# Optimization experiments

Hardware: AMD Instinct MI355X
Metric: run time of the kernel (lower is better)

Reference implementation:

```python
import jax, jax.numpy as jnp
import numpy as np

B, T, C = 1, 2048, 1024
H = 16
D = C // H
FF = 4 * C


def layernorm(x, g, b, eps=1e-5):
    mu = jnp.mean(x, axis=-1, keepdims=True)
    var = jnp.var(x, axis=-1, keepdims=True)
    return (x - mu) * jax.lax.rsqrt(var + eps) * g + b


def setup_inputs() -> dict:
    key = jax.random.key(0)
    ks = jax.random.split(key, 16)
    s = 0.02
    return {
        "x": jax.random.normal(ks[0], (B, T, C), jnp.float32),
        "qkv_w": jax.random.normal(ks[1], (C, 3 * C), jnp.float32) * s,
        "qkv_b": jnp.zeros((3 * C,), jnp.float32),
        "out_w": jax.random.normal(ks[2], (C, C), jnp.float32) * s,
        "out_b": jnp.zeros((C,), jnp.float32),
        "ln1_g": jnp.ones((C,), jnp.float32),
        "ln1_b": jnp.zeros((C,), jnp.float32),
        "ln2_g": jnp.ones((C,), jnp.float32),
        "ln2_b": jnp.zeros((C,), jnp.float32),
        "w1": jax.random.normal(ks[3], (C, FF), jnp.float32) * s,
        "b1": jnp.zeros((FF,), jnp.float32),
        "w2": jax.random.normal(ks[4], (FF, C), jnp.float32) * s,
        "b2": jnp.zeros((C,), jnp.float32),
    }


def linear_attention(h, qkv_w, qkv_b, out_w, out_b):
    qkv = h @ qkv_w + qkv_b                      # (B,T,3C)
    q, k, v = jnp.split(qkv, 3, axis=-1)
    # (B,T,C) -> (B,H,T,D)
    reshape = lambda a: a.reshape(B, T, H, D).transpose(0, 2, 1, 3)
    q, k, v = reshape(q), reshape(k), reshape(v)
    Q = jax.nn.elu(q) + 1.0
    K = jax.nn.elu(k) + 1.0
    # causal linear attention via cumulative outer-products
    KV = jnp.einsum('bhtd,bhte->bhtde', K, v)    # (B,H,T,D,D)
    KV_cum = jnp.cumsum(KV, axis=2)
    K_cum = jnp.cumsum(K, axis=2)
    num = jnp.einsum('bhtd,bhtde->bhte', Q, KV_cum)
    den = jnp.einsum('bhtd,bhtd->bht', Q, K_cum)[..., None]
    o = num / (den + 1e-6)                       # (B,H,T,D)
    o = o.transpose(0, 2, 1, 3).reshape(B, T, C)
    return o @ out_w + out_b


def reference(x, qkv_w, qkv_b, out_w, out_b, ln1_g, ln1_b, ln2_g, ln2_b, w1, b1, w2, b2):
    x = x + linear_attention(layernorm(x, ln1_g, ln1_b), qkv_w, qkv_b, out_w, out_b)
    h = layernorm(x, ln2_g, ln2_b)
    mlp = jax.nn.gelu(h @ w1 + b1, approximate=False) @ w2 + b2
    return x + mlp
```

## Files before the change

kernel.cpp:

```cpp
#include <hip/hip_runtime.h>

typedef unsigned short u16;
typedef __bf16 bf16x8 __attribute__((ext_vector_type(8)));
typedef float f32x4 __attribute__((ext_vector_type(4)));
typedef unsigned short u16x8 __attribute__((ext_vector_type(8)));
typedef unsigned short u16x4 __attribute__((ext_vector_type(4)));

__device__ __forceinline__ float bf2f(u16 u){
  union { unsigned i; float f; } v; v.i = ((unsigned)u) << 16; return v.f;
}
__device__ __forceinline__ u16 f2bf(float f){
  union { float f; unsigned i; } v; v.f = f;
  unsigned r = v.i + 0x7FFFu + ((v.i >> 16) & 1u);
  return (u16)(r >> 16);
}
__device__ __forceinline__ float elup(float x){ return x > 0.f ? x + 1.f : expf(x); }

__device__ __forceinline__ void gload_lds16(const void* gsrc, void* ldst){
  __builtin_amdgcn_global_load_lds(
      (__attribute__((address_space(1))) void*)(unsigned long long)gsrc,
      (__attribute__((address_space(3))) void*)(unsigned)(unsigned long long)ldst,
      16, 0, 0);
}

struct TD { const float* in; u16* out; int R, Cc, cx, ntiles; };

__global__ __launch_bounds__(256) void prep(TD d0, TD d1, TD d2, TD d3,
                                            const float* __restrict__ x, const float* __restrict__ g,
                                            const float* __restrict__ b, u16* __restrict__ y){
  __shared__ u16 tile[32][33];
  __shared__ float ls[4], ls2[4];
  int bidx = blockIdx.x, tid = threadIdx.x;
  if (bidx >= 12288){
    int row = bidx - 12288;
    size_t base = (size_t)row*1024 + tid*4;
    f32x4 xv = *(const f32x4*)(x + base);
    float v0=xv[0], v1=xv[1], v2=xv[2], v3=xv[3];
    float s  = v0+v1+v2+v3;
    float s2 = v0*v0+v1*v1+v2*v2+v3*v3;
    #pragma unroll
    for (int off=32; off>0; off>>=1){ s += __shfl_xor(s, off); s2 += __shfl_xor(s2, off); }
    if ((tid & 63) == 0){ ls[tid>>6] = s; ls2[tid>>6] = s2; }
    __syncthreads();
    float ts = ls[0]+ls[1]+ls[2]+ls[3];
    float ts2 = ls2[0]+ls2[1]+ls2[2]+ls2[3];
    float mean = ts*(1.f/1024.f);
    float var  = ts2*(1.f/1024.f) - mean*mean;
    float rstd = rsqrtf(var + 1e-5f);
    f32x4 gv = *(const f32x4*)(g + tid*4);
    f32x4 bv = *(const f32x4*)(b + tid*4);
    u16x4 ov;
    ov[0]=f2bf((v0-mean)*rstd*gv[0]+bv[0]);
    ov[1]=f2bf((v1-mean)*rstd*gv[1]+bv[1]);
    ov[2]=f2bf((v2-mean)*rstd*gv[2]+bv[2]);
    ov[3]=f2bf((v3-mean)*rstd*gv[3]+bv[3]);
    *(u16x4*)(y + base) = ov;
    return;
  }
  int bb = bidx;
  TD d;
  if (bb < d0.ntiles) d = d0;
  else { bb -= d0.ntiles;
    if (bb < d1.ntiles) d = d1;
    else { bb -= d1.ntiles;
      if (bb < d2.ntiles) d = d2;
      else { bb -= d2.ntiles; d = d3; } } }
  int c0 = (bb % d.cx) * 32, r0 = (bb / d.cx) * 32;
  int tx = tid & 31, ty = tid >> 5;
  #pragma unroll
  for (int i=0;i<4;i++)
    tile[ty + i*8][tx] = f2bf(d.in[(size_t)(r0 + ty + i*8)*d.Cc + c0 + tx]);
  __syncthreads();
  #pragma unroll
  for (int i=0;i<4;i++)
    d.out[(size_t)(c0 + ty + i*8)*d.R + r0 + tx] = tile[tx][ty + i*8];
}

__global__ __launch_bounds__(256) void ln2_fused(const u16* __restrict__ P0, const u16* __restrict__ P1,
                                                 const u16* __restrict__ P2, const u16* __restrict__ P3,
                                                 const float* __restrict__ bias, const float* __restrict__ xres,
                                                 const float* __restrict__ g, const float* __restrict__ b,
                                                 float* __restrict__ x2, u16* __restrict__ h2){
  int row = blockIdx.x, tid = threadIdx.x;
  size_t base = (size_t)row*1024 + tid*4;
  u16x4 a0 = *(const u16x4*)(P0 + base);
  u16x4 a1 = *(const u16x4*)(P1 + base);
  u16x4 a2 = *(const u16x4*)(P2 + base);
  u16x4 a3 = *(const u16x4*)(P3 + base);
  f32x4 rv = *(const f32x4*)(xres + base);
  f32x4 bv = *(const f32x4*)(bias + tid*4);
  f32x4 v;
  #pragma unroll
  for (int j=0;j<4;j++) v[j] = (bf2f(a0[j])+bf2f(a1[j])) + (bf2f(a2[j])+bf2f(a3[j])) + bv[j] + rv[j];
  *(f32x4*)(x2 + base) = v;
  float s  = v[0]+v[1]+v[2]+v[3];
  float s2 = v[0]*v[0]+v[1]*v[1]+v[2]*v[2]+v[3]*v[3];
  #pragma unroll
  for (int off=32; off>0; off>>=1){ s += __shfl_xor(s, off); s2 += __shfl_xor(s2, off); }
  __shared__ float ls[4], ls2[4];
  if ((tid & 63) == 0){ ls[tid>>6] = s; ls2[tid>>6] = s2; }
  __syncthreads();
  float ts = ls[0]+ls[1]+ls[2]+ls[3];
  float ts2 = ls2[0]+ls2[1]+ls2[2]+ls2[3];
  float mean = ts*(1.f/1024.f);
  float var  = ts2*(1.f/1024.f) - mean*mean;
  float rstd = rsqrtf(var + 1e-5f);
  f32x4 gv = *(const f32x4*)(g + tid*4);
  f32x4 bb = *(const f32x4*)(b + tid*4);
  u16x4 ov;
  #pragma unroll
  for (int j=0;j<4;j++) ov[j] = f2bf((v[j]-mean)*rstd*gv[j]+bb[j]);
  *(u16x4*)(h2 + base) = ov;
}

template<int EPI>
__global__ __launch_bounds__(512, 4) void gemm_bt(const u16* __restrict__ A, const u16* __restrict__ BT,
                                                  const float* __restrict__ bias, const float* __restrict__ res,
                                                  void* __restrict__ out, int N, int K, size_t pstride){
  __shared__ u16 As[2][128*64];
  __shared__ u16 Bs[2][128*64];
  int tid = threadIdx.x;
  int w = tid >> 6, lane = tid & 63;
  int m0 = blockIdx.x * 128, n0 = blockIdx.y * 128;
  int Kc = K / gridDim.z;
  int kbase = blockIdx.z * Kc;
  int nt = Kc / 64;

  f32x4 acc[2][4] = {};

  int l3 = lane >> 3, l7 = lane & 7;
  const u16* aSrc = A  + (size_t)(m0 + w*16 + l3)*K + kbase + (l7 ^ l3)*8;
  const u16* bSrc = BT + (size_t)(n0 + w*16 + l3)*K + kbase + (l7 ^ l3)*8;
  int r0 = (w>>1)*32, c0 = (w&1)*64;
  int lrow = lane & 15, g4 = lane >> 4;
  int swz = (lrow & 7) << 4;

  {
    u16* aD = As[0] + w*16*64;
    u16* bD = Bs[0] + w*16*64;
    gload_lds16(aSrc,                aD);
    gload_lds16(aSrc + (size_t)8*K,  aD + 8*64);
    gload_lds16(bSrc,                bD);
    gload_lds16(bSrc + (size_t)8*K,  bD + 8*64);
  }
  __syncthreads();

  int cur = 0;
  for (int t = 0; t < nt; ++t){
    if (t + 1 < nt){
      int k0 = (t+1)*64;
      u16* aD = As[cur^1] + w*16*64;
      u16* bD = Bs[cur^1] + w*16*64;
      gload_lds16(aSrc + k0,               aD);
      gload_lds16(aSrc + (size_t)8*K + k0, aD + 8*64);
      gload_lds16(bSrc + k0,               bD);
      gload_lds16(bSrc + (size_t)8*K + k0, bD + 8*64);
    }
    const char* Ab = (const char*)As[cur];
    const char* Bb = (const char*)Bs[cur];
    #pragma unroll
    for (int kk=0; kk<2; kk++){
      int ko = (kk*64 + g4*16) ^ swz;
      bf16x8 af[2], bfv[4];
      #pragma unroll
      for (int mi=0;mi<2;mi++) af[mi]  = *(const bf16x8*)(Ab + (r0 + mi*16 + lrow)*128 + ko);
      #pragma unroll
      for (int ni=0;ni<4;ni++) bfv[ni] = *(const bf16x8*)(Bb + (c0 + ni*16 + lrow)*128 + ko);
      #pragma unroll
      for (int mi=0;mi<2;mi++)
        #pragma unroll
        for (int ni=0;ni<4;ni++)
          acc[mi][ni] = __builtin_amdgcn_mfma_f32_16x16x32_bf16(af[mi], bfv[ni], acc[mi][ni], 0, 0, 0);
    }
    __syncthreads();
    cur ^= 1;
  }

  int lgr = lane >> 4;
  u16* pout = (EPI == 3) ? ((u16*)out + (size_t)blockIdx.z * pstride) : (u16*)out;
  #pragma unroll
  for (int mi=0;mi<2;mi++){
    #pragma unroll
    for (int j=0;j<4;j++){
      int row = m0 + r0 + mi*16 + lgr*4 + j;
      #pragma unroll
      for (int ni=0;ni<4;ni++){
        int col = n0 + c0 + ni*16 + lrow;
        size_t idx = (size_t)row*N + col;
        if constexpr (EPI == 3){
          pout[idx] = f2bf(acc[mi][ni][j]);
        } else {
          float v = acc[mi][ni][j] + bias[col];
          if constexpr (EPI == 0){
            ((u16*)out)[idx] = f2bf(v);
          } else {
            v = 0.5f * v * (1.f + erff(v * 0.70710678118654752f));
            ((u16*)out)[idx] = f2bf(v);
          }
        }
      }
    }
  }
}

__global__ __launch_bounds__(256) void reduce4(const u16* __restrict__ P0, const u16* __restrict__ P1,
                                               const u16* __restrict__ P2, const u16* __restrict__ P3,
                                               const float* __restrict__ bias, const float* __restrict__ res,
                                               float* __restrict__ out){
  size_t i = ((size_t)blockIdx.x*256 + threadIdx.x)*4;
  u16x4 a = *(const u16x4*)(P0 + i);
  u16x4 b = *(const u16x4*)(P1 + i);
  u16x4 c = *(const u16x4*)(P2 + i);
  u16x4 d = *(const u16x4*)(P3 + i);
  f32x4 rv = *(const f32x4*)(res + i);
  f32x4 bv = *(const f32x4*)(bias + (i & 1023));
  f32x4 o;
  #pragma unroll
  for (int j=0;j<4;j++) o[j] = (bf2f(a[j]) + bf2f(b[j])) + (bf2f(c[j]) + bf2f(d[j])) + bv[j] + rv[j];
  *(f32x4*)(out + i) = o;
}

__global__ __launch_bounds__(256) void attn_chunksum(const u16* __restrict__ qkv, float* __restrict__ S,
                                                     float* __restrict__ Ks){
  __shared__ u16 KT[64*72];
  __shared__ u16 VT[64*72];
  int c = blockIdx.x, h = blockIdx.y, tid = threadIdx.x;
  int t = tid >> 2, seg = tid & 3, e0 = seg*16;
  size_t rowb = (size_t)(c*64 + t)*3072 + h*64 + e0;
  u16x8 k0 = *(const u16x8*)(qkv + rowb + 1024);
  u16x8 k1 = *(const u16x8*)(qkv + rowb + 1032);
  u16x8 v0 = *(const u16x8*)(qkv + rowb + 2048);
  u16x8 v1 = *(const u16x8*)(qkv + rowb + 2056);
  #pragma unroll
  for (int i=0;i<8;i++){
    KT[(e0 + i)*72 + t]     = f2bf(elup(bf2f(k0[i])));
    KT[(e0 + 8 + i)*72 + t] = f2bf(elup(bf2f(k1[i])));
    VT[(e0 + i)*72 + t]     = v0[i];
    VT[(e0 + 8 + i)*72 + t] = v1[i];
  }
  __syncthreads();

  int w = tid >> 6, lane = tid & 63;
  int lr = lane & 15, lk = (lane>>4)*8, g = lane >> 4, cl = lane & 15;
  bf16x8 av_[2];
  #pragma unroll
  for (int kk=0;kk<2;kk++) av_[kk] = *(const bf16x8*)(VT + (w*16 + lr)*72 + kk*32 + lk);
  f32x4 acc[4] = {};
  #pragma unroll
  for (int di=0;di<4;di++){
    #pragma unroll
    for (int kk=0;kk<2;kk++){
      bf16x8 bk = *(const bf16x8*)(KT + (di*16 + lr)*72 + kk*32 + lk);
      acc[di] = __builtin_amdgcn_mfma_f32_16x16x32_bf16(av_[kk], bk, acc[di], 0, 0, 0);
    }
  }
  size_t base = (size_t)(h*32 + c)*4096;
  #pragma unroll
  for (int di=0;di<4;di++)
    #pragma unroll
    for (int j=0;j<4;j++)
      S[base + (size_t)(w*16 + g*4 + j)*64 + di*16 + cl] = acc[di][j];

  float s = 0.f;
  #pragma unroll
  for (int i=0;i<16;i++) s += bf2f(KT[t*72 + e0 + i]);
  s += __shfl_xor(s, 1); s += __shfl_xor(s, 2);
  if (seg == 0) Ks[(size_t)(h*32 + c)*64 + t] = s;
}

__global__ __launch_bounds__(256) void attn_prefix(float* __restrict__ S, float* __restrict__ Ks){
  int g = blockIdx.x, h = blockIdx.y, tid = threadIdx.x;
  size_t hb = (size_t)h * 32 * 4096;
  int idx = g*256 + tid;
  float run = 0.f;
  for (int c=0; c<32; c++){
    size_t p = hb + (size_t)c*4096 + idx;
    float v = S[p]; S[p] = run; run += v;
  }
  if (g == 0 && tid < 64){
    float r2 = 0.f;
    for (int c=0; c<32; c++){
      size_t p = (size_t)(h*32 + c)*64 + tid;
      float v = Ks[p]; Ks[p] = r2; r2 += v;
    }
  }
}

__global__ __launch_bounds__(256) void attn_out(const u16* __restrict__ qkv, const float* __restrict__ S,
                                                const float* __restrict__ Ks, u16* __restrict__ o){
  __shared__ u16 Qs [64*72];
  __shared__ u16 Ksh[64*72];
  __shared__ u16 VT [64*72];
  __shared__ u16 SpT[64*72];
  __shared__ u16 Am [64*72];
  __shared__ float kp[64], den[64];
  int c = blockIdx.x, h = blockIdx.y, tid = threadIdx.x;
  int t = tid >> 2, seg = tid & 3, e0 = seg*16;

  size_t rowb = (size_t)(c*64 + t)*3072 + h*64 + e0;
  u16x8 q0 = *(const u16x8*)(qkv + rowb);
  u16x8 q1 = *(const u16x8*)(qkv + rowb + 8);
  u16x8 k0 = *(const u16x8*)(qkv + rowb + 1024);
  u16x8 k1 = *(const u16x8*)(qkv + rowb + 1032);
  u16x8 v0 = *(const u16x8*)(qkv + rowb + 2048);
  u16x8 v1 = *(const u16x8*)(qkv + rowb + 2056);
  #pragma unroll
  for (int i=0;i<8;i++){
    Qs [t*72 + e0 + i]     = f2bf(elup(bf2f(q0[i])));
    Qs [t*72 + e0 + 8 + i] = f2bf(elup(bf2f(q1[i])));
    Ksh[t*72 + e0 + i]     = f2bf(elup(bf2f(k0[i])));
    Ksh[t*72 + e0 + 8 + i] = f2bf(elup(bf2f(k1[i])));
    VT [(e0 + i)*72 + t]     = v0[i];
    VT [(e0 + 8 + i)*72 + t] = v1[i];
  }
  size_t sbase = (size_t)(h*32 + c)*4096;
  {
    const f32x4* sp = (const f32x4*)(S + sbase + (size_t)t*64 + e0);
    #pragma unroll
    for (int qd=0;qd<4;qd++){
      f32x4 v = sp[qd];
      #pragma unroll
      for (int j=0;j<4;j++) SpT[t*72 + e0 + qd*4 + j] = f2bf(v[j]);
    }
  }
  if (tid < 64) kp[tid] = Ks[(size_t)(h*32 + c)*64 + tid];
  __syncthreads();

  int w = tid >> 6, lane = tid & 63;
  int lr = lane & 15, lk = (lane>>4)*8, g = lane >> 4, cl = lane & 15;

  bf16x8 aq[2];
  #pragma unroll
  for (int kk=0;kk<2;kk++) aq[kk] = *(const bf16x8*)(Qs + (w*16 + lr)*72 + kk*32 + lk);

  f32x4 acc[4] = {};
  #pragma unroll
  for (int ni=0;ni<4;ni++){
    #pragma unroll
    for (int kk=0;kk<2;kk++){
      bf16x8 bs = *(const bf16x8*)(SpT + (ni*16 + lr)*72 + kk*32 + lk);
      acc[ni] = __builtin_amdgcn_mfma_f32_16x16x32_bf16(aq[kk], bs, acc[ni], 0, 0, 0);
    }
  }
  #pragma unroll
  for (int si=0;si<4;si++){
    f32x4 qk = {};
    #pragma unroll
    for (int kk=0;kk<2;kk++){
      bf16x8 bk = *(const bf16x8*)(Ksh + (si*16 + lr)*72 + kk*32 + lk);
      qk = __builtin_amdgcn_mfma_f32_16x16x32_bf16(aq[kk], bk, qk, 0, 0, 0);
    }
    #pragma unroll
    for (int j=0;j<4;j++){
      int rowt = w*16 + g*4 + j;
      int scol = si*16 + cl;
      Am[rowt*72 + scol] = f2bf((scol <= rowt) ? qk[j] : 0.f);
    }
  }
  __syncthreads();

  {
    float dsum = 0.f;
    #pragma unroll
    for (int i=0;i<16;i++) dsum += bf2f(Am[t*72 + e0 + i]);
    #pragma unroll
    for (int i=0;i<16;i++) dsum += bf2f(Qs[t*72 + e0 + i]) * kp[e0 + i];
    dsum += __shfl_xor(dsum, 1); dsum += __shfl_xor(dsum, 2);
    if (seg == 0) den[t] = dsum;
  }
  {
    bf16x8 aa[2];
    #pragma unroll
    for (int kk=0;kk<2;kk++) aa[kk] = *(const bf16x8*)(Am + (w*16 + lr)*72 + kk*32 + lk);
    #pragma unroll
    for (int ni=0;ni<4;ni++){
      #pragma unroll
      for (int kk=0;kk<2;kk++){
        bf16x8 bv = *(const bf16x8*)(VT + (ni*16 + lr)*72 + kk*32 + lk);
        acc[ni] = __builtin_amdgcn_mfma_f32_16x16x32_bf16(aa[kk], bv, acc[ni], 0, 0, 0);
      }
    }
  }
  __syncthreads();

  #pragma unroll
  for (int j=0;j<4;j++){
    int rowt = w*16 + g*4 + j;
    float inv = 1.f/(den[rowt] + 1e-6f);
    #pragma unroll
    for (int ni=0;ni<4;ni++)
      o[(size_t)(c*64 + rowt)*1024 + h*64 + ni*16 + cl] = f2bf(acc[ni][j]*inv);
  }
}

extern "C" void kernel_launch(void* const* d_in, const int* in_sizes, int n_in,
                              void* d_out, int out_size, void* d_ws, size_t ws_size,
                              hipStream_t stream) {
  (void)in_sizes; (void)n_in; (void)out_size; (void)ws_size;
  const float* x     = (const float*)d_in[0];
  const float* qkv_w = (const float*)d_in[1];
  const float* qkv_b = (const float*)d_in[2];
  const float* out_w = (const float*)d_in[3];
  const float* out_b = (const float*)d_in[4];
  const float* ln1_g = (const float*)d_in[5];
  const float* ln1_b = (const float*)d_in[6];
  const float* ln2_g = (const float*)d_in[7];
  const float* ln2_b = (const float*)d_in[8];
  const float* w1    = (const float*)d_in[9];
  const float* b1    = (const float*)d_in[10];
  const float* w2    = (const float*)d_in[11];
  const float* b2    = (const float*)d_in[12];

  char* ws = (char*)d_ws;
  u16*   wT_qkv = (u16*)  (ws);
  u16*   wT_out = (u16*)  (ws +  6291456);
  u16*   wT_w1  = (u16*)  (ws +  8388608);
  u16*   wT_w2  = (u16*)  (ws + 16777216);
  u16*   h1     = (u16*)  (ws + 25165824);
  u16*   qkv    = (u16*)  (ws + 29360128);
  float* Ssum   = (float*)(ws + 41943040);
  float* ksum   = (float*)(ws + 50331648);
  float* x2     = (float*)(ws + 50462720);
  u16*   h2     = (u16*)  (ws + 58851328);
  u16*   o      = h1;
  u16*   a1     = qkv;
  u16*   Pa0    = (u16*)(ws + 29360128);
  size_t PaStride = 2097152;
  u16*   Pm0    = (u16*)(ws);
  u16*   Pm1    = (u16*)(ws +  4194304);
  u16*   Pm2    = (u16*)(ws +  8388608);
  u16*   Pm3    = (u16*)(ws + 12582912);
  size_t PmStride = 2097152;
  float* outp   = (float*)d_out;

  TD t0{qkv_w, wT_qkv, 1024, 3072,  96, 3072};
  TD t1{out_w, wT_out, 1024, 1024,  32, 1024};
  TD t2{w1,    wT_w1,  1024, 4096, 128, 4096};
  TD t3{w2,    wT_w2,  4096, 1024,  32, 4096};
  prep<<<14336, 256, 0, stream>>>(t0, t1, t2, t3, x, ln1_g, ln1_b, h1);

  gemm_bt<0><<<dim3(16, 24, 1), 512, 0, stream>>>(h1, wT_qkv, qkv_b, nullptr, qkv, 3072, 1024, 0);

  attn_chunksum<<<dim3(32, 16), 256, 0, stream>>>(qkv, Ssum, ksum);
  attn_prefix  <<<dim3(16, 16), 256, 0, stream>>>(Ssum, ksum);
  attn_out     <<<dim3(32, 16), 256, 0, stream>>>(qkv, Ssum, ksum, o);

  gemm_bt<3><<<dim3(16, 8, 4), 512, 0, stream>>>(o, wT_out, nullptr, nullptr, Pa0, 1024, 1024, PaStride);
  ln2_fused<<<2048, 256, 0, stream>>>(Pa0, Pa0 + PaStride, Pa0 + 2*PaStride, Pa0 + 3*PaStride,
                                      out_b, x, ln2_g, ln2_b, x2, h2);

  gemm_bt<1><<<dim3(16, 32, 1), 512, 0, stream>>>(h2, wT_w1, b1, nullptr, a1, 4096, 1024, 0);

  gemm_bt<3><<<dim3(16, 8, 4), 512, 0, stream>>>(a1, wT_w2, nullptr, nullptr, Pm0, 1024, 4096, PmStride);
  reduce4<<<2048, 256, 0, stream>>>(Pm0, Pm1, Pm2, Pm3, b2, x2, outp);
}
```

Baseline: 129.4 us.

## Add triple-buffered GEMM pipeline and fold chunk prefix sum into attn_out

The GEMM kernel is templated on pipeline depth. A 3-stage variant uses manual vmcnt waits, one barrier per k-step and s_setprio around the MFMA compute, and it is applied to the out-proj, W1 and W2 GEMMs. The separate attn_prefix kernel is removed. Each attn_out block now sums the preceding chunk states itself, which saves a launch and a read-modify-write pass over S but adds redundant reads that grow linearly with the chunk index. The deeper pipeline raises LDS use per block to 96KB, which may reduce occupancy.

After: 149.6 us. +15.7%, slower.

```diff
diff --git a/kernel.cpp b/kernel.cpp
--- a/kernel.cpp
+++ b/kernel.cpp
@@ -113,12 +113,12 @@
   *(u16x4*)(h2 + base) = ov;
 }
 
-template<int EPI>
+template<int EPI, int DEPTH>
 __global__ __launch_bounds__(512, 4) void gemm_bt(const u16* __restrict__ A, const u16* __restrict__ BT,
                                                   const float* __restrict__ bias, const float* __restrict__ res,
                                                   void* __restrict__ out, int N, int K, size_t pstride){
-  __shared__ u16 As[2][128*64];
-  __shared__ u16 Bs[2][128*64];
+  __shared__ u16 As[DEPTH][128*64];
+  __shared__ u16 Bs[DEPTH][128*64];
   int tid = threadIdx.x;
   int w = tid >> 6, lane = tid & 63;
   int m0 = blockIdx.x * 128, n0 = blockIdx.y * 128;
@@ -135,29 +135,18 @@
   int lrow = lane & 15, g4 = lane >> 4;
   int swz = (lrow & 7) << 4;
 
-  {
-    u16* aD = As[0] + w*16*64;
-    u16* bD = Bs[0] + w*16*64;
-    gload_lds16(aSrc,                aD);
-    gload_lds16(aSrc + (size_t)8*K,  aD + 8*64);
-    gload_lds16(bSrc,                bD);
-    gload_lds16(bSrc + (size_t)8*K,  bD + 8*64);
-  }
-  __syncthreads();
-
-  int cur = 0;
-  for (int t = 0; t < nt; ++t){
-    if (t + 1 < nt){
-      int k0 = (t+1)*64;
-      u16* aD = As[cur^1] + w*16*64;
-      u16* bD = Bs[cur^1] + w*16*64;
-      gload_lds16(aSrc + k0,               aD);
-      gload_lds16(aSrc + (size_t)8*K + k0, aD + 8*64);
-      gload_lds16(bSrc + k0,               bD);
-      gload_lds16(bSrc + (size_t)8*K + k0, bD + 8*64);
-    }
-    const char* Ab = (const char*)As[cur];
-    const char* Bb = (const char*)Bs[cur];
+  auto STAGE = [&](int kt, int buf){
+    u16* aD = As[buf] + w*16*64;
+    u16* bD = Bs[buf] + w*16*64;
+    int k0 = kt*64;
+    gload_lds16(aSrc + k0,               aD);
+    gload_lds16(aSrc + (size_t)8*K + k0, aD + 8*64);
+    gload_lds16(bSrc + k0,               bD);
+    gload_lds16(bSrc + (size_t)8*K + k0, bD + 8*64);
+  };
+  auto COMPUTE = [&](int buf){
+    const char* Ab = (const char*)As[buf];
+    const char* Bb = (const char*)Bs[buf];
     #pragma unroll
     for (int kk=0; kk<2; kk++){
       int ko = (kk*64 + g4*16) ^ swz;
@@ -172,8 +161,37 @@
         for (int ni=0;ni<4;ni++)
           acc[mi][ni] = __builtin_amdgcn_mfma_f32_16x16x32_bf16(af[mi], bfv[ni], acc[mi][ni], 0, 0, 0);
     }
+  };
+
+  if constexpr (DEPTH == 2){
+    STAGE(0, 0);
     __syncthreads();
-    cur ^= 1;
+    int cur = 0;
+    for (int t = 0; t < nt; ++t){
+      if (t + 1 < nt) STAGE(t+1, cur^1);
+      COMPUTE(cur);
+      __syncthreads();
+      cur ^= 1;
+    }
+  } else {
+    STAGE(0, 0); STAGE(1, 1);
+    int cur = 0;
+    for (int t = 0; t < nt-1; ++t){
+      asm volatile("s_waitcnt vmcnt(4)" ::: "memory");
+      __builtin_amdgcn_s_barrier();
+      __builtin_amdgcn_sched_barrier(0);
+      int nb = cur + 2; if (nb >= 3) nb -= 3;
+      if (t + 2 < nt) STAGE(t+2, nb);
+      __builtin_amdgcn_s_setprio(1);
+      COMPUTE(cur);
+      __builtin_amdgcn_s_setprio(0);
+      int c1 = cur + 1; if (c1 >= 3) c1 -= 3;
+      cur = c1;
+    }
+    asm volatile("s_waitcnt vmcnt(0)" ::: "memory");
+    __builtin_amdgcn_s_barrier();
+    __builtin_amdgcn_sched_barrier(0);
+    COMPUTE(cur);
   }
 
   int lgr = lane >> 4;
@@ -268,24 +286,6 @@
   if (seg == 0) Ks[(size_t)(h*32 + c)*64 + t] = s;
 }
 
-__global__ __launch_bounds__(256) void attn_prefix(float* __restrict__ S, float* __restrict__ Ks){
-  int g = blockIdx.x, h = blockIdx.y, tid = threadIdx.x;
-  size_t hb = (size_t)h * 32 * 4096;
-  int idx = g*256 + tid;
-  float run = 0.f;
-  for (int c=0; c<32; c++){
-    size_t p = hb + (size_t)c*4096 + idx;
-    float v = S[p]; S[p] = run; run += v;
-  }
-  if (g == 0 && tid < 64){
-    float r2 = 0.f;
-    for (int c=0; c<32; c++){
-      size_t p = (size_t)(h*32 + c)*64 + tid;
-      float v = Ks[p]; Ks[p] = r2; r2 += v;
-    }
-  }
-}
-
 __global__ __launch_bounds__(256) void attn_out(const u16* __restrict__ qkv, const float* __restrict__ S,
                                                 const float* __restrict__ Ks, u16* __restrict__ o){
   __shared__ u16 Qs [64*72];
@@ -313,17 +313,25 @@
     VT [(e0 + i)*72 + t]     = v0[i];
     VT [(e0 + 8 + i)*72 + t] = v1[i];
   }
-  size_t sbase = (size_t)(h*32 + c)*4096;
   {
-    const f32x4* sp = (const f32x4*)(S + sbase + (size_t)t*64 + e0);
-    #pragma unroll
-    for (int qd=0;qd<4;qd++){
-      f32x4 v = sp[qd];
-      #pragma unroll
-      for (int j=0;j<4;j++) SpT[t*72 + e0 + qd*4 + j] = f2bf(v[j]);
-    }
-  }
-  if (tid < 64) kp[tid] = Ks[(size_t)(h*32 + c)*64 + tid];
+    f32x4 sa0={}, sa1={}, sa2={}, sa3={};
+    for (int cc=0; cc<c; cc++){
+      const f32x4* sp = (const f32x4*)(S + (size_t)(h*32 + cc)*4096 + (size_t)t*64 + e0);
+      sa0 += sp[0]; sa1 += sp[1]; sa2 += sp[2]; sa3 += sp[3];
+    }
+    #pragma unroll
+    for (int j=0;j<4;j++){
+      SpT[t*72 + e0 + j]      = f2bf(sa0[j]);
+      SpT[t*72 + e0 + 4 + j]  = f2bf(sa1[j]);
+      SpT[t*72 + e0 + 8 + j]  = f2bf(sa2[j]);
+      SpT[t*72 + e0 + 12 + j] = f2bf(sa3[j]);
+    }
+  }
+  if (tid < 64){
+    float k = 0.f;
+    for (int cc=0; cc<c; cc++) k += Ks[(size_t)(h*32 + cc)*64 + tid];
+    kp[tid] = k;
+  }
   __syncthreads();
 
   int w = tid >> 6, lane = tid & 63;
@@ -439,18 +447,17 @@
   TD t3{w2,    wT_w2,  4096, 1024,  32, 4096};
   prep<<<14336, 256, 0, stream>>>(t0, t1, t2, t3, x, ln1_g, ln1_b, h1);
 
-  gemm_bt<0><<<dim3(16, 24, 1), 512, 0, stream>>>(h1, wT_qkv, qkv_b, nullptr, qkv, 3072, 1024, 0);
+  gemm_bt<0,2><<<dim3(16, 24, 1), 512, 0, stream>>>(h1, wT_qkv, qkv_b, nullptr, qkv, 3072, 1024, 0);
 
   attn_chunksum<<<dim3(32, 16), 256, 0, stream>>>(qkv, Ssum, ksum);
-  attn_prefix  <<<dim3(16, 16), 256, 0, stream>>>(Ssum, ksum);
   attn_out     <<<dim3(32, 16), 256, 0, stream>>>(qkv, Ssum, ksum, o);
 
-  gemm_bt<3><<<dim3(16, 8, 4), 512, 0, stream>>>(o, wT_out, nullptr, nullptr, Pa0, 1024, 1024, PaStride);
+  gemm_bt<3,3><<<dim3(16, 8, 4), 512, 0, stream>>>(o, wT_out, nullptr, nullptr, Pa0, 1024, 1024, PaStride);
   ln2_fused<<<2048, 256, 0, stream>>>(Pa0, Pa0 + PaStride, Pa0 + 2*PaStride, Pa0 + 3*PaStride,
                                       out_b, x, ln2_g, ln2_b, x2, h2);
 
-  gemm_bt<1><<<dim3(16, 32, 1), 512, 0, stream>>>(h2, wT_w1, b1, nullptr, a1, 4096, 1024, 0);
-
-  gemm_bt<3><<<dim3(16, 8, 4), 512, 0, stream>>>(a1, wT_w2, nullptr, nullptr, Pm0, 1024, 4096, PmStride);
+  gemm_bt<1,3><<<dim3(16, 32, 1), 512, 0, stream>>>(h2, wT_w1, b1, nullptr, a1, 4096, 1024, 0);
+
+  gemm_bt<3,3><<<dim3(16, 8, 4), 512, 0, stream>>>(a1, wT_w2, nullptr, nullptr, Pm0, 1024, 4096, PmStride);
   reduce4<<<2048, 256, 0, stream>>>(Pm0, Pm1, Pm2, Pm3, b2, x2, outp);
 }
```

## Fold chunk prefix scan into attn_out and drop separate prefix kernel

Applied to the files above, without the earlier changes.

Removes the attn_prefix launch and has each attn_out block sum the chunk states of all earlier chunks directly, computing its own exclusive prefix of S and Ks. Blocks are launched in reverse chunk order so the heaviest blocks (late chunks, most summation) start first. This saves one kernel launch and a read-modify-write pass over S. In exchange, total reads of S grow quadratically with chunk count (up to 31 chunk states per block), and the per-block load becomes unbalanced.

Measured after the change: 142.0 us. 9.8% more time.

```diff
diff --git a/kernel.cpp b/kernel.cpp
--- a/kernel.cpp
+++ b/kernel.cpp
@@ -268,24 +268,6 @@
   if (seg == 0) Ks[(size_t)(h*32 + c)*64 + t] = s;
 }
 
-__global__ __launch_bounds__(256) void attn_prefix(float* __restrict__ S, float* __restrict__ Ks){
-  int g = blockIdx.x, h = blockIdx.y, tid = threadIdx.x;
-  size_t hb = (size_t)h * 32 * 4096;
-  int idx = g*256 + tid;
-  float run = 0.f;
-  for (int c=0; c<32; c++){
-    size_t p = hb + (size_t)c*4096 + idx;
-    float v = S[p]; S[p] = run; run += v;
-  }
-  if (g == 0 && tid < 64){
-    float r2 = 0.f;
-    for (int c=0; c<32; c++){
-      size_t p = (size_t)(h*32 + c)*64 + tid;
-      float v = Ks[p]; Ks[p] = r2; r2 += v;
-    }
-  }
-}
-
 __global__ __launch_bounds__(256) void attn_out(const u16* __restrict__ qkv, const float* __restrict__ S,
                                                 const float* __restrict__ Ks, u16* __restrict__ o){
   __shared__ u16 Qs [64*72];
@@ -294,7 +276,7 @@
   __shared__ u16 SpT[64*72];
   __shared__ u16 Am [64*72];
   __shared__ float kp[64], den[64];
-  int c = blockIdx.x, h = blockIdx.y, tid = threadIdx.x;
+  int c = 31 - blockIdx.x, h = blockIdx.y, tid = threadIdx.x;
   int t = tid >> 2, seg = tid & 3, e0 = seg*16;
 
   size_t rowb = (size_t)(c*64 + t)*3072 + h*64 + e0;
@@ -313,17 +295,25 @@
     VT [(e0 + i)*72 + t]     = v0[i];
     VT [(e0 + 8 + i)*72 + t] = v1[i];
   }
-  size_t sbase = (size_t)(h*32 + c)*4096;
   {
-    const f32x4* sp = (const f32x4*)(S + sbase + (size_t)t*64 + e0);
-    #pragma unroll
-    for (int qd=0;qd<4;qd++){
-      f32x4 v = sp[qd];
-      #pragma unroll
-      for (int j=0;j<4;j++) SpT[t*72 + e0 + qd*4 + j] = f2bf(v[j]);
-    }
-  }
-  if (tid < 64) kp[tid] = Ks[(size_t)(h*32 + c)*64 + tid];
+    f32x4 sa0={}, sa1={}, sa2={}, sa3={};
+    for (int cc=0; cc<c; cc++){
+      const f32x4* sp = (const f32x4*)(S + (size_t)(h*32 + cc)*4096 + (size_t)t*64 + e0);
+      sa0 += sp[0]; sa1 += sp[1]; sa2 += sp[2]; sa3 += sp[3];
+    }
+    #pragma unroll
+    for (int j=0;j<4;j++){
+      SpT[t*72 + e0 + j]      = f2bf(sa0[j]);
+      SpT[t*72 + e0 + 4 + j]  = f2bf(sa1[j]);
+      SpT[t*72 + e0 + 8 + j]  = f2bf(sa2[j]);
+      SpT[t*72 + e0 + 12 + j] = f2bf(sa3[j]);
+    }
+  }
+  if (tid < 64){
+    float k = 0.f;
+    for (int cc=0; cc<c; cc++) k += Ks[(size_t)(h*32 + cc)*64 + tid];
+    kp[tid] = k;
+  }
   __syncthreads();
 
   int w = tid >> 6, lane = tid & 63;
@@ -442,7 +432,6 @@
   gemm_bt<0><<<dim3(16, 24, 1), 512, 0, stream>>>(h1, wT_qkv, qkv_b, nullptr, qkv, 3072, 1024, 0);
 
   attn_chunksum<<<dim3(32, 16), 256, 0, stream>>>(qkv, Ssum, ksum);
-  attn_prefix  <<<dim3(16, 16), 256, 0, stream>>>(Ssum, ksum);
   attn_out     <<<dim3(32, 16), 256, 0, stream>>>(qkv, Ssum, ksum, o);
 
   gemm_bt<3><<<dim3(16, 8, 4), 512, 0, stream>>>(o, wT_out, nullptr, nullptr, Pa0, 1024, 1024, PaStride);
```
